# Performance work log

Hardware: AMD Instinct MI355X
Metric: run time of the kernel (lower is better)

Reference implementation:

```python
import jax, jax.numpy as jnp
import numpy as np

D_MODEL = 1024
NUM_HEADS = 16
HEAD_DIM = D_MODEL // NUM_HEADS
B, T = 2, 2048


def setup_inputs() -> dict:
    key = jax.random.key(0)
    kx, kq, kk, kv, ko = jax.random.split(key, 5)
    s = 1.0 / np.sqrt(D_MODEL)
    x = jax.random.normal(kx, (B, T, D_MODEL), dtype=jnp.float32)
    Wq = jax.random.normal(kq, (D_MODEL, D_MODEL), dtype=jnp.float32) * s
    Wk = jax.random.normal(kk, (D_MODEL, D_MODEL), dtype=jnp.float32) * s
    Wv = jax.random.normal(kv, (D_MODEL, D_MODEL), dtype=jnp.float32) * s
    Wo = jax.random.normal(ko, (D_MODEL, D_MODEL), dtype=jnp.float32) * s
    # causal boolean mask [T,T], True = keep (every row keeps >=1 key)
    attn_mask = jnp.tril(jnp.ones((T, T), dtype=bool))
    return {"x": x, "Wq": Wq, "Wk": Wk, "Wv": Wv, "Wo": Wo, "attn_mask": attn_mask}


def reference(x, Wq, Wk, Wv, Wo, attn_mask):
    Bb, Tt, Dd = x.shape
    h, dh = NUM_HEADS, HEAD_DIM
    # Linear(bias=False): y = x @ W.T
    q = (x @ Wq.T).reshape(Bb, Tt, h, dh).transpose(0, 2, 1, 3)  # [B,h,T,dh]
    k = (x @ Wk.T).reshape(Bb, Tt, h, dh).transpose(0, 2, 1, 3)
    v = (x @ Wv.T).reshape(Bb, Tt, h, dh).transpose(0, 2, 1, 3)
    scores = jnp.einsum('bhqd,bhkd->bhqk', q, k) / jnp.sqrt(jnp.float32(dh))
    keep = attn_mask[None, None, :, :]  # [1,1,T,T], True = keep
    scores = jnp.where(keep, scores, -jnp.inf)
    # original subtracts row max then softmax; jax.nn.softmax is equivalent (stable)
    attn = jax.nn.softmax(scores, axis=-1)
    out = jnp.einsum('bhqk,bhkd->bhqd', attn, v)  # [B,h,T,dh]
    out = out.transpose(0, 2, 1, 3).reshape(Bb, Tt, Dd)
    return out @ Wo.T
```

## Files before the change

kernel.cpp:

```cpp
#include <hip/hip_runtime.h>
#include <hip/hip_bf16.h>
#include <stdint.h>

typedef __bf16 bf16_t;
typedef bf16_t bf16x8 __attribute__((ext_vector_type(8)));
typedef float  f32x4  __attribute__((ext_vector_type(4)));
typedef float  f32x16 __attribute__((ext_vector_type(16)));

#define MFMA16(a, b, c) __builtin_amdgcn_mfma_f32_16x16x32_bf16((a), (b), (c), 0, 0, 0)
#define MFMA32(a, b, c) __builtin_amdgcn_mfma_f32_32x32x16_bf16((a), (b), (c), 0, 0, 0)

static __device__ __forceinline__ unsigned short f2bf(float f) {
    __hip_bfloat16 h = __float2bfloat16(f);
    return __builtin_bit_cast(unsigned short, h);
}
static __device__ __forceinline__ unsigned int pk2(float a, float b) {
    return ((unsigned int)f2bf(b) << 16) | (unsigned int)f2bf(a);
}

static __device__ __forceinline__ void gld_lds16(const void* g, void* l) {
    __builtin_amdgcn_global_load_lds(
        (const __attribute__((address_space(1))) uint32_t*)g,
        (__attribute__((address_space(3))) uint32_t*)l, 16, 0, 0);
}

#define TT     2048
#define DM     1024
#define NH     16
#define HD     64

__global__ __launch_bounds__(256) void cast_x(const float* __restrict__ src,
                                              unsigned short* __restrict__ dst, int n4) {
    int i = blockIdx.x * 256 + threadIdx.x;
    if (i >= n4) return;
    float4 v = reinterpret_cast<const float4*>(src)[i];
    ushort4 o;
    o.x = f2bf(v.x); o.y = f2bf(v.y); o.z = f2bf(v.z); o.w = f2bf(v.w);
    reinterpret_cast<ushort4*>(dst)[i] = o;
}

__global__ __launch_bounds__(256) void cast_w(const float* __restrict__ wq,
                                              const float* __restrict__ wk,
                                              const float* __restrict__ wv,
                                              const float* __restrict__ wo_in,
                                              unsigned short* __restrict__ wqkv,
                                              unsigned short* __restrict__ wo_out) {
    const int y = blockIdx.y;
    const float* src = (y == 0) ? wq : (y == 1) ? wk : (y == 2) ? wv : wo_in;
    unsigned short* dst = (y < 3) ? (wqkv + (size_t)y * (1u << 20)) : wo_out;
    int i = blockIdx.x * 256 + threadIdx.x;
    float4 v = reinterpret_cast<const float4*>(src)[i];
    ushort4 o;
    o.x = f2bf(v.x); o.y = f2bf(v.y); o.z = f2bf(v.z); o.w = f2bf(v.w);
    reinterpret_cast<ushort4*>(dst)[i] = o;
}

template <int BM, int BN, int WM, int WN, int MODE>
__global__ __launch_bounds__(512, 1)
void gemm4d(const unsigned short* __restrict__ A, const unsigned short* __restrict__ W,
            float* __restrict__ out, int Nn,
            unsigned short* __restrict__ qp, unsigned short* __restrict__ kp,
            unsigned short* __restrict__ vp, int gridM) {
    constexpr int THREADS = WM * WN * 64;
    static_assert(THREADS == 512, "template assumes 512 threads");
    constexpr int MF = BM / WM / 16;
    constexpr int NF = BN / WN / 16;
    constexpr int ABYTES = BM * 64;
    constexpr int BUFB = ABYTES + BN * 64;
    constexpr int APT = BM / 128;
    constexpr int BPT = BN / 128;
    constexpr int IPT = APT + BPT;
    extern __shared__ char lds[];

    const int tid = threadIdx.x;
    const int l = tid & 63, w = tid >> 6;
    const int r = l & 15, g = l >> 4;
    const int wm = w / WN, wn = w % WN;

    const int bid = blockIdx.x;
    const int cpx = gridDim.x >> 3;
    const int swz = (bid & 7) * cpx + (bid >> 3);
    const int m0 = (swz % gridM) * BM;
    const int n0 = (swz / gridM) * BN;

    const int srow = tid >> 2;
    const int gcol = (tid & 3) ^ (srow & 3);
    const unsigned short* aG = A + (size_t)(m0 + srow) * 1024 + gcol * 8;
    const unsigned short* bG = W + (size_t)(n0 + srow) * 1024 + gcol * 8;

#define STAGE4(buf, t)                                                         \
    do {                                                                       \
        char* ab_ = lds + (buf) * BUFB;                                        \
        char* bb_ = ab_ + ABYTES;                                              \
        _Pragma("unroll")                                                      \
        for (int q_ = 0; q_ < APT; ++q_)                                       \
            gld_lds16(aG + (size_t)q_ * 128 * 1024 + (t) * 32,                 \
                      ab_ + q_ * 8192 + tid * 16);                             \
        _Pragma("unroll")                                                      \
        for (int q_ = 0; q_ < BPT; ++q_)                                       \
            gld_lds16(bG + (size_t)q_ * 128 * 1024 + (t) * 32,                 \
                      bb_ + q_ * 8192 + tid * 16);                             \
    } while (0)

    f32x4 acc[MF][NF];
#pragma unroll
    for (int i = 0; i < MF; i++)
#pragma unroll
        for (int j = 0; j < NF; j++) acc[i][j] = (f32x4){0.f, 0.f, 0.f, 0.f};

    STAGE4(0, 0);
    STAGE4(1, 1);
    STAGE4(2, 2);

    const int rdsw = ((g ^ (r & 3)) << 4);

    for (int t = 0; t < 32; ++t) {
        if constexpr (IPT == 4) {
            if (t <= 29)      asm volatile("s_waitcnt vmcnt(8)" ::: "memory");
            else if (t == 30) asm volatile("s_waitcnt vmcnt(4)" ::: "memory");
            else              asm volatile("s_waitcnt vmcnt(0)" ::: "memory");
        } else {
            if (t <= 29)      asm volatile("s_waitcnt vmcnt(4)" ::: "memory");
            else if (t == 30) asm volatile("s_waitcnt vmcnt(2)" ::: "memory");
            else              asm volatile("s_waitcnt vmcnt(0)" ::: "memory");
        }
        __builtin_amdgcn_sched_barrier(0);
        __builtin_amdgcn_s_barrier();
        __builtin_amdgcn_sched_barrier(0);

        const char* ab_ = lds + (t & 3) * BUFB;
        const char* bb_ = ab_ + ABYTES;
        bf16x8 af[MF], bfr[NF];
#pragma unroll
        for (int i = 0; i < MF; ++i)
            af[i] = *reinterpret_cast<const bf16x8*>(
                ab_ + (wm * (BM / WM) + i * 16 + r) * 64 + rdsw);
#pragma unroll
        for (int j = 0; j < NF; ++j)
            bfr[j] = *reinterpret_cast<const bf16x8*>(
                bb_ + (wn * (BN / WN) + j * 16 + r) * 64 + rdsw);

        if (t < 29) STAGE4((t + 3) & 3, t + 3);

        __builtin_amdgcn_s_setprio(1);
#pragma unroll
        for (int i = 0; i < MF; ++i)
#pragma unroll
            for (int j = 0; j < NF; ++j) acc[i][j] = MFMA16(af[i], bfr[j], acc[i][j]);
        __builtin_amdgcn_s_setprio(0);
    }
#undef STAGE4

#pragma unroll
    for (int i = 0; i < MF; ++i) {
#pragma unroll
        for (int j = 0; j < NF; ++j) {
#pragma unroll
            for (int reg = 0; reg < 4; ++reg) {
                const int mg = m0 + wm * (BM / WM) + i * 16 + g * 4 + reg;
                const int ng = n0 + wn * (BN / WN) + j * 16 + r;
                const float v = acc[i][j][reg];
                if constexpr (MODE == 1) {
                    out[(size_t)mg * Nn + ng] = v;
                } else {
                    const int sel = ng >> 10;
                    const int c10 = ng & 1023;
                    const int h = c10 >> 6, d = c10 & 63;
                    const int bb2 = mg >> 11, tq = mg & 2047;
                    const int bh = bb2 * NH + h;
                    if (sel == 0)      qp[(bh * TT + tq) * HD + d] = f2bf(v * 0.125f);
                    else if (sel == 1) kp[(bh * TT + tq) * HD + d] = f2bf(v);
                    else               vp[(bh * HD + d) * TT + tq] = f2bf(v);
                }
            }
        }
    }
}

__global__ __launch_bounds__(256) void attn_kernel(const unsigned short* __restrict__ q,
                                                   const unsigned short* __restrict__ k,
                                                   const unsigned short* __restrict__ v,
                                                   unsigned short* __restrict__ o) {
    __shared__ unsigned short lK[64 * 64];
    __shared__ unsigned short lV[64 * 64];

    const int tid = threadIdx.x;
    const int l   = tid & 63;
    const int w   = tid >> 6;
    const int c   = l & 31;
    const int hi  = l >> 5;

    const int id   = blockIdx.x;
    const int half = id >> 8;
    const int sub  = id & 255;
    const int bh   = sub >> 3;
    const int j8   = sub & 7;
    const int qt   = half ? (15 - j8) : j8;
    const int q0w  = qt * 128 + w * 32;
    const int nkt  = 2 * qt + 2;

    const unsigned short* qbase = q + (size_t)bh * TT * HD;
    const unsigned short* kbase = k + (size_t)bh * TT * HD;
    const unsigned short* vbase = v + (size_t)bh * HD * TT;

    bf16x8 qf[4];
#pragma unroll
    for (int ks = 0; ks < 4; ++ks)
        qf[ks] = *reinterpret_cast<const bf16x8*>(qbase + (q0w + c) * HD + ks * 16 + hi * 8);

    f32x16 Oacc[2];
#pragma unroll
    for (int jd = 0; jd < 2; ++jd)
#pragma unroll
        for (int e = 0; e < 16; ++e) Oacc[jd][e] = 0.f;
    float m_r = -1e30f, l_r = 0.f;

    const int cA = tid, cB = tid + 256;
    const int rA = cA >> 3, colA = (cA & 7) * 8;
    const int rB = cB >> 3, colB = (cB & 7) * 8;
    const int dstA = rA * 128 + ((colA * 2) ^ ((rA & 7) << 4));
    const int dstB = rB * 128 + ((colB * 2) ^ ((rB & 7) << 4));

    uint4 ka, kb, va, vb;
    ka = *reinterpret_cast<const uint4*>(kbase + rA * HD + colA);
    kb = *reinterpret_cast<const uint4*>(kbase + rB * HD + colB);
    va = *reinterpret_cast<const uint4*>(vbase + rA * TT + colA);
    vb = *reinterpret_cast<const uint4*>(vbase + rB * TT + colB);

    for (int kt = 0; kt < nkt; ++kt) {
        const int k0 = kt * 64;
        __syncthreads();
        *reinterpret_cast<uint4*>((char*)lK + dstA) = ka;
        *reinterpret_cast<uint4*>((char*)lK + dstB) = kb;
        *reinterpret_cast<uint4*>((char*)lV + dstA) = va;
        *reinterpret_cast<uint4*>((char*)lV + dstB) = vb;
        __syncthreads();
        if (kt + 1 < nkt) {
            const int kn = k0 + 64;
            ka = *reinterpret_cast<const uint4*>(kbase + (kn + rA) * HD + colA);
            kb = *reinterpret_cast<const uint4*>(kbase + (kn + rB) * HD + colB);
            va = *reinterpret_cast<const uint4*>(vbase + rA * TT + kn + colA);
            vb = *reinterpret_cast<const uint4*>(vbase + rB * TT + kn + colB);
        }
        if (k0 > q0w + 31) continue;

        f32x16 s[2];
#pragma unroll
        for (int j = 0; j < 2; ++j) {
#pragma unroll
            for (int e = 0; e < 16; ++e) s[j][e] = 0.f;
#pragma unroll
            for (int ks = 0; ks < 4; ++ks) {
                const int row = j * 32 + c;
                bf16x8 kf = *reinterpret_cast<const bf16x8*>(
                    (char*)lK + row * 128 + (((ks * 16 + hi * 8) * 2) ^ ((row & 7) << 4)));
                s[j] = MFMA32(kf, qf[ks], s[j]);
            }
        }

        if (k0 + 63 > q0w) {
            const int qg = q0w + c;
#pragma unroll
            for (int j = 0; j < 2; ++j)
#pragma unroll
                for (int e = 0; e < 16; ++e) {
                    const int kv = k0 + j * 32 + (e & 3) + 8 * (e >> 2) + 4 * hi;
                    if (kv > qg) s[j][e] = -1e30f;
                }
        }

        float mx = s[0][0];
#pragma unroll
        for (int e = 1; e < 16; ++e) mx = fmaxf(mx, s[0][e]);
#pragma unroll
        for (int e = 0; e < 16; ++e) mx = fmaxf(mx, s[1][e]);
        mx = fmaxf(mx, __shfl_xor(mx, 32));
        const float mnew = fmaxf(m_r, mx);
        const float corr = __expf(m_r - mnew);
        float sum = 0.f;
#pragma unroll
        for (int j = 0; j < 2; ++j)
#pragma unroll
            for (int e = 0; e < 16; ++e) {
                const float p = __expf(s[j][e] - mnew);
                s[j][e] = p;
                sum += p;
            }
        sum += __shfl_xor(sum, 32);
        l_r = l_r * corr + sum;
        m_r = mnew;
#pragma unroll
        for (int jd = 0; jd < 2; ++jd)
#pragma unroll
            for (int e = 0; e < 16; ++e) Oacc[jd][e] *= corr;

        bf16x8 pa[4];
#pragma unroll
        for (int ks = 0; ks < 4; ++ks) {
            const int j = ks >> 1;
            const int base = (ks & 1) * 8;
            const unsigned int pA0 = pk2(s[j][base + 0], s[j][base + 1]);
            const unsigned int pA1 = pk2(s[j][base + 2], s[j][base + 3]);
            const unsigned int pB0 = pk2(s[j][base + 4], s[j][base + 5]);
            const unsigned int pB1 = pk2(s[j][base + 6], s[j][base + 7]);
            const unsigned int m0_ = hi ? pB0 : pA0;
            const unsigned int m1_ = hi ? pB1 : pA1;
            const unsigned int o0 = hi ? pA0 : pB0;
            const unsigned int o1 = hi ? pA1 : pB1;
            const unsigned int r0 = __shfl_xor(o0, 32);
            const unsigned int r1 = __shfl_xor(o1, 32);
            uint4 u;
            u.x = hi ? r0 : m0_;
            u.y = hi ? r1 : m1_;
            u.z = hi ? m0_ : r0;
            u.w = hi ? m1_ : r1;
            pa[ks] = __builtin_bit_cast(bf16x8, u);
        }

#pragma unroll
        for (int jd = 0; jd < 2; ++jd) {
#pragma unroll
            for (int ks = 0; ks < 4; ++ks) {
                const int row = jd * 32 + c;
                bf16x8 vf = *reinterpret_cast<const bf16x8*>(
                    (char*)lV + row * 128 + (((ks * 16 + hi * 8) * 2) ^ ((row & 7) << 4)));
                Oacc[jd] = MFMA32(vf, pa[ks], Oacc[jd]);
            }
        }
    }

    const int b_ = bh >> 4, h_ = bh & 15;
    const float inv = 1.f / l_r;
    const int qg = q0w + c;
    unsigned short* orow = o + ((size_t)b_ * TT + qg) * DM + h_ * HD;
#pragma unroll
    for (int jd = 0; jd < 2; ++jd)
#pragma unroll
        for (int ep = 0; ep < 8; ++ep) {
            const int e0 = ep * 2;
            const int d0 = jd * 32 + (e0 & 3) + 8 * (e0 >> 2) + 4 * hi;
            const unsigned int pkv = pk2(Oacc[jd][e0] * inv, Oacc[jd][e0 + 1] * inv);
            *reinterpret_cast<unsigned int*>(orow + d0) = pkv;
        }
}

extern "C" void kernel_launch(void* const* d_in, const int* in_sizes, int n_in,
                              void* d_out, int out_size, void* d_ws, size_t ws_size,
                              hipStream_t stream) {
    const float* x  = (const float*)d_in[0];
    const float* Wq = (const float*)d_in[1];
    const float* Wk = (const float*)d_in[2];
    const float* Wv = (const float*)d_in[3];
    const float* Wo = (const float*)d_in[4];

    char* ws = (char*)d_ws;
    unsigned short* xb   = (unsigned short*)(ws);
    unsigned short* wqkv = (unsigned short*)(ws + (8u  << 20));
    unsigned short* wo   = (unsigned short*)(ws + (14u << 20));
    unsigned short* qb   = (unsigned short*)(ws + (16u << 20));
    unsigned short* kb   = (unsigned short*)(ws + (24u << 20));
    unsigned short* vb   = (unsigned short*)(ws + (32u << 20));
    unsigned short* ab   = (unsigned short*)(ws + (40u << 20));
    float* outp = (float*)d_out;

    cast_x<<<4096, 256, 0, stream>>>(x, xb, 1048576);
    cast_w<<<dim3(1024, 4), 256, 0, stream>>>(Wq, Wk, Wv, Wo, wqkv, wo);

    gemm4d<256, 256, 2, 4, 0><<<192, 512, 131072, stream>>>(
        xb, wqkv, nullptr, 3072, qb, kb, vb, 16);
    attn_kernel<<<512, 256, 0, stream>>>(qb, kb, vb, ab);
    gemm4d<128, 128, 4, 2, 1><<<256, 512, 65536, stream>>>(
        ab, wo, outp, 1024, nullptr, nullptr, nullptr, 32);
}
```

Measured before the change: 219.9 us.

## Read V directly from global in attention and add direct-B output projection GEMM

```diff
diff --git a/kernel.cpp b/kernel.cpp
--- a/kernel.cpp
+++ b/kernel.cpp
@@ -177,12 +177,77 @@
     }
 }
 
+__global__ __launch_bounds__(512, 1)
+void gemm_bd(const unsigned short* __restrict__ A, const unsigned short* __restrict__ W,
+             float* __restrict__ out) {
+    __shared__ char lds[2][8192];
+
+    const int tid = threadIdx.x;
+    const int l = tid & 63, w = tid >> 6;
+    const int r = l & 15, g = l >> 4;
+    const int wm = w >> 2, wn = w & 3;
+
+    const int bid = blockIdx.x;
+    const int swz = (bid & 7) * 32 + (bid >> 3);
+    const int m0 = (swz & 31) * 128;
+    const int n0 = (swz >> 5) * 128;
+
+    const int srow = tid >> 2;
+    const int gcol = (tid & 3) ^ (srow & 3);
+    const unsigned short* aG = A + (size_t)(m0 + srow) * 1024 + gcol * 8;
+    const int rdsw = ((g ^ (r & 3)) << 4);
+
+    const unsigned short* bGd = W + (size_t)(n0 + wn * 32 + r) * 1024 + g * 8;
+
+    f32x4 acc[4][2];
+#pragma unroll
+    for (int i = 0; i < 4; i++)
+#pragma unroll
+        for (int j = 0; j < 2; j++) acc[i][j] = (f32x4){0.f, 0.f, 0.f, 0.f};
+
+    gld_lds16(aG, &lds[0][tid * 16]);
+    __syncthreads();
+
+    for (int t = 0; t < 32; ++t) {
+        bf16x8 bfr[2];
+#pragma unroll
+        for (int j = 0; j < 2; ++j)
+            bfr[j] = *reinterpret_cast<const bf16x8*>(bGd + (size_t)j * 16 * 1024 + t * 32);
+
+        if (t + 1 < 32) gld_lds16(aG + (t + 1) * 32, &lds[(t + 1) & 1][tid * 16]);
+
+        const char* ab_ = lds[t & 1];
+        bf16x8 af[4];
+#pragma unroll
+        for (int i = 0; i < 4; ++i)
+            af[i] = *reinterpret_cast<const bf16x8*>(ab_ + (wm * 64 + i * 16 + r) * 64 + rdsw);
+
+        __builtin_amdgcn_s_setprio(1);
+#pragma unroll
+        for (int i = 0; i < 4; ++i)
+#pragma unroll
+            for (int j = 0; j < 2; ++j) acc[i][j] = MFMA16(af[i], bfr[j], acc[i][j]);
+        __builtin_amdgcn_s_setprio(0);
+        __syncthreads();
+    }
+
+#pragma unroll
+    for (int i = 0; i < 4; ++i)
+#pragma unroll
+        for (int j = 0; j < 2; ++j)
+#pragma unroll
+            for (int reg = 0; reg < 4; ++reg) {
+                const int mg = m0 + wm * 64 + i * 16 + g * 4 + reg;
+                const int ng = n0 + wn * 32 + j * 16 + r;
+                out[(size_t)mg * DM + ng] = acc[i][j][reg];
+            }
+}
+
 __global__ __launch_bounds__(256) void attn_kernel(const unsigned short* __restrict__ q,
                                                    const unsigned short* __restrict__ k,
                                                    const unsigned short* __restrict__ v,
                                                    unsigned short* __restrict__ o) {
     __shared__ unsigned short lK[64 * 64];
-    __shared__ unsigned short lV[64 * 64];
 
     const int tid = threadIdx.x;
     const int l   = tid & 63;
@@ -221,26 +286,20 @@
     const int dstA = rA * 128 + ((colA * 2) ^ ((rA & 7) << 4));
     const int dstB = rB * 128 + ((colB * 2) ^ ((rB & 7) << 4));
 
-    uint4 ka, kb, va, vb;
+    uint4 ka, kb;
     ka = *reinterpret_cast<const uint4*>(kbase + rA * HD + colA);
     kb = *reinterpret_cast<const uint4*>(kbase + rB * HD + colB);
-    va = *reinterpret_cast<const uint4*>(vbase + rA * TT + colA);
-    vb = *reinterpret_cast<const uint4*>(vbase + rB * TT + colB);
 
     for (int kt = 0; kt < nkt; ++kt) {
         const int k0 = kt * 64;
         __syncthreads();
         *reinterpret_cast<uint4*>((char*)lK + dstA) = ka;
         *reinterpret_cast<uint4*>((char*)lK + dstB) = kb;
-        *reinterpret_cast<uint4*>((char*)lV + dstA) = va;
-        *reinterpret_cast<uint4*>((char*)lV + dstB) = vb;
         __syncthreads();
         if (kt + 1 < nkt) {
             const int kn = k0 + 64;
             ka = *reinterpret_cast<const uint4*>(kbase + (kn + rA) * HD + colA);
             kb = *reinterpret_cast<const uint4*>(kbase + (kn + rB) * HD + colB);
-            va = *reinterpret_cast<const uint4*>(vbase + rA * TT + kn + colA);
-            vb = *reinterpret_cast<const uint4*>(vbase + rB * TT + kn + colB);
         }
         if (k0 > q0w + 31) continue;
 
@@ -321,9 +380,8 @@
         for (int jd = 0; jd < 2; ++jd) {
 #pragma unroll
             for (int ks = 0; ks < 4; ++ks) {
-                const int row = jd * 32 + c;
                 bf16x8 vf = *reinterpret_cast<const bf16x8*>(
-                    (char*)lV + row * 128 + (((ks * 16 + hi * 8) * 2) ^ ((row & 7) << 4)));
+                    vbase + (size_t)(jd * 32 + c) * TT + k0 + ks * 16 + hi * 8);
                 Oacc[jd] = MFMA32(vf, pa[ks], Oacc[jd]);
             }
         }
@@ -369,6 +427,5 @@
     gemm4d<256, 256, 2, 4, 0><<<192, 512, 131072, stream>>>(
         xb, wqkv, nullptr, 3072, qb, kb, vb, 16);
     attn_kernel<<<512, 256, 0, stream>>>(qb, kb, vb, ab);
-    gemm4d<128, 128, 4, 2, 1><<<256, 512, 65536, stream>>>(
-        ab, wo, outp, 1024, nullptr, nullptr, nullptr, 32);
-}
+    gemm_bd<<<256, 512, 0, stream>>>(ab, wo, outp);
+}
```

Measured after the change: 269.5 us. 1.23x slower.
